# Optimization experiments

Hardware: AMD Instinct MI355X
Metric: run time of the kernel (lower is better)

The kernel has to match this reference:

```python
import jax, jax.numpy as jnp
import numpy as np

N = 50000
D = 256
E = 800000


def setup_inputs() -> dict:
    key = jax.random.key(0)
    ks = jax.random.split(key, 8)
    x = jax.random.normal(ks[0], (N, D), dtype=jnp.float32)
    edge_index = jax.random.randint(ks[1], (2, E), 0, N, dtype=jnp.int64)
    s = 1.0 / np.sqrt(D)
    # SAGEConv layer 0 params: lin_l (neighbors, with bias), lin_r (root, no bias)
    Wl0 = jax.random.uniform(ks[2], (D, D), jnp.float32, -s, s)
    bl0 = jnp.zeros((D,), jnp.float32)
    Wr0 = jax.random.uniform(ks[3], (D, D), jnp.float32, -s, s)
    # SAGEConv layer 1 params
    Wl1 = jax.random.uniform(ks[4], (D, D), jnp.float32, -s, s)
    bl1 = jnp.zeros((D,), jnp.float32)
    Wr1 = jax.random.uniform(ks[5], (D, D), jnp.float32, -s, s)
    return {"x": x, "edge_index": edge_index, "Wl0": Wl0, "bl0": bl0, "Wr0": Wr0,
            "Wl1": Wl1, "bl1": bl1, "Wr1": Wr1}


def _sage_conv(x, edge_index, Wl, bl, Wr):
    # PyG SAGEConv, aggr='mean': out = lin_l(mean_{j in N(i)} x_j) + lin_r(x_i)
    src, dst = edge_index[0], edge_index[1]
    msg = x[src]                                            # [E, D] gather
    agg = jax.ops.segment_sum(msg, dst, num_segments=x.shape[0])
    cnt = jax.ops.segment_sum(jnp.ones((edge_index.shape[1],), x.dtype), dst,
                              num_segments=x.shape[0])
    mean = agg / jnp.maximum(cnt, 1.0)[:, None]             # zero-degree -> 0
    return mean @ Wl + bl + x @ Wr


def reference(x, edge_index, Wl0, bl0, Wr0, Wl1, bl1, Wr1):
    negative_slope = 0.5
    target = x  # full-graph path: target nodes = all nodes
    h = x
    # dropout p=0.0 -> identity
    h = _sage_conv(h, edge_index, Wl0, bl0, Wr0)
    h = jnp.where(h >= 0, h, negative_slope * h)
    h = _sage_conv(h, edge_index, Wl1, bl1, Wr1)
    h = jnp.where(h >= 0, h, negative_slope * h)
    return (h, target)
```

## Files before the change

kernel.cpp:

```cpp
#include <hip/hip_runtime.h>
#include <hip/hip_fp8.h>


typedef __attribute__((ext_vector_type(8))) short bf16x8;
typedef __attribute__((ext_vector_type(4))) float f32x4;

__device__ __forceinline__ float bf2f(unsigned short b) {
    union { unsigned u; float f; } x; x.u = ((unsigned)b) << 16; return x.f;
}
__device__ __forceinline__ short f2bf(float f) {
    union { float f; unsigned u; } x; x.f = f;
    unsigned r = x.u + 0x7fffu + ((x.u >> 16) & 1u);
    return (short)(r >> 16);
}
__device__ __forceinline__ unsigned char f2fp8(float f) {
    __hip_fp8_e4m3 q(f);
    return (unsigned char)q.__x;
}
__device__ __forceinline__ float fp82f(unsigned char b) {
    __hip_fp8_e4m3 q; q.__x = (__hip_fp8_storage_t)b;
    return (float)q;
}

#define BINA_CHUNK 8192


__global__ __launch_bounds__(512) void bkhist_prep_kernel(
    const int* __restrict__ ei, int* __restrict__ hist, int E, int NBK, int NCH,
    const float* __restrict__ x, short* __restrict__ xb,
    unsigned char* __restrict__ xq, float* __restrict__ xcopy,
    const float* __restrict__ Wl0, const float* __restrict__ Wr0,
    const float* __restrict__ Wl1, const float* __restrict__ Wr1,
    short* __restrict__ B1T, short* __restrict__ B2T, int total8) {
    if ((int)blockIdx.x < NCH) {
        __shared__ int h[512];
        int c = blockIdx.x;
        int base_e = c * BINA_CHUNK;
        int nloc = E - base_e;
        if (nloc > BINA_CHUNK) nloc = BINA_CHUNK;
        for (int b = threadIdx.x; b < 512; b += 512) h[b] = 0;
        __syncthreads();
        for (int t = threadIdx.x; t < nloc; t += 512)
            atomicAdd(&h[ei[E + base_e + t] >> 7], 1);
        __syncthreads();
        if ((int)threadIdx.x < NBK) hist[c * 512 + threadIdx.x] = h[threadIdx.x];
    } else {
        int gid = ((int)blockIdx.x - NCH) * 512 + threadIdx.x;
        if (gid < total8) {
            const float* p = x + (size_t)gid * 8;
            float4 v0 = *reinterpret_cast<const float4*>(p);
            float4 v1 = *reinterpret_cast<const float4*>(p + 4);
            bf16x8 t;
            t[0] = f2bf(v0.x); t[1] = f2bf(v0.y); t[2] = f2bf(v0.z); t[3] = f2bf(v0.w);
            t[4] = f2bf(v1.x); t[5] = f2bf(v1.y); t[6] = f2bf(v1.z); t[7] = f2bf(v1.w);
            *reinterpret_cast<bf16x8*>(xb + (size_t)gid * 8) = t;
            uchar4 q0, q1;
            q0.x = f2fp8(v0.x); q0.y = f2fp8(v0.y); q0.z = f2fp8(v0.z); q0.w = f2fp8(v0.w);
            q1.x = f2fp8(v1.x); q1.y = f2fp8(v1.y); q1.z = f2fp8(v1.z); q1.w = f2fp8(v1.w);
            *reinterpret_cast<uchar4*>(xq + (size_t)gid * 8) = q0;
            *reinterpret_cast<uchar4*>(xq + (size_t)gid * 8 + 4) = q1;
            *reinterpret_cast<float4*>(xcopy + (size_t)gid * 8) = v0;
            *reinterpret_cast<float4*>(xcopy + (size_t)gid * 8 + 4) = v1;
        } else {
            int idx = gid - total8;
            if (idx < 262144) {
                int sel = idx >> 17;
                int j = idx & 131071;
                int n = j >> 9;
                int k = j & 511;
                const float* Wl = sel ? Wl1 : Wl0;
                const float* Wr = sel ? Wr1 : Wr0;
                float v = (k < 256) ? Wl[k * 256 + n] : Wr[(k - 256) * 256 + n];
                (sel ? B2T : B1T)[j] = f2bf(v);
            }
        }
    }
}

__global__ __launch_bounds__(512) void bkscan_kernel(
    int* __restrict__ hist, int* __restrict__ bkoff, int* __restrict__ offs,
    int NBK, int NCH, int N, int E) {
    __shared__ int sm[512];
    int b = threadIdx.x;
    int run = 0;
    if (b < NBK) {
        for (int c = 0; c < NCH; ++c) {
            int h = hist[c * 512 + b];
            hist[c * 512 + b] = run;
            run += h;
        }
    }
    sm[b] = run;
    __syncthreads();
    for (int off = 1; off < 512; off <<= 1) {
        int t = (b >= off) ? sm[b - off] : 0;
        __syncthreads();
        sm[b] += t;
        __syncthreads();
    }
    int excl = sm[b] - run;
    if (b < NBK) {
        bkoff[b] = excl;
        for (int c = 0; c < NCH; ++c) hist[c * 512 + b] += excl;
    }
    if (b == 0) {
        bkoff[NBK] = E;
        offs[N] = E;
    }
}


__global__ __launch_bounds__(512) void binA_kernel(
    const int* __restrict__ ei, const int* __restrict__ hist,
    long long* __restrict__ pairs, int E, int NBK) {
    __shared__ int pos[512];
    int c = blockIdx.x;
    if ((int)threadIdx.x < NBK) pos[threadIdx.x] = hist[c * 512 + threadIdx.x];
    __syncthreads();
    int base_e = c * BINA_CHUNK;
    int nloc = E - base_e;
    if (nloc > BINA_CHUNK) nloc = BINA_CHUNK;
    for (int t = threadIdx.x; t < nloc; t += 512) {
        int dst = ei[E + base_e + t];
        int src = ei[base_e + t];
        int p = atomicAdd(&pos[dst >> 7], 1);
        pairs[p] = ((long long)dst << 32) | (unsigned)src;
    }
}


__global__ __launch_bounds__(256) void binB_kernel(
    const long long* __restrict__ pairs, const int* __restrict__ bkoff,
    int* __restrict__ offs, float* __restrict__ invdeg,
    int* __restrict__ csr, int NBK, int N) {
    __shared__ int cnt[128];
    __shared__ int cur[128];
    int b = blockIdx.x;
    int t = threadIdx.x;
    if (t < 128) cnt[t] = 0;
    __syncthreads();
    int beg = bkoff[b];
    int end = bkoff[b + 1];
    for (int i = beg + t; i < end; i += 256)
        atomicAdd(&cnt[((int)(pairs[i] >> 32)) & 127], 1);
    __syncthreads();
    if (t < 64) {
        int c0 = cnt[2 * t], c1 = cnt[2 * t + 1];
        int s = c0 + c1;
        int incl = s;
        #pragma unroll
        for (int d = 1; d < 64; d <<= 1) {
            int x = __shfl_up(incl, d, 64);
            if (t >= d) incl += x;
        }
        int excl = incl - s;
        cur[2 * t] = beg + excl;
        cur[2 * t + 1] = beg + excl + c0;
    }
    __syncthreads();
    if (t < 128) {
        int node = (b << 7) + t;
        if (node < N) {
            offs[node] = cur[t];
            invdeg[node] = 1.0f / (float)(cnt[t] > 0 ? cnt[t] : 1);
        }
    }
    __syncthreads();
    for (int i = beg + t; i < end; i += 256) {
        long long p = pairs[i];
        int pos = atomicAdd(&cur[((int)(p >> 32)) & 127], 1);
        csr[pos] = (int)(p & 0xffffffffLL);
    }
}

__global__ __launch_bounds__(256) void agg_kernel(
    const unsigned char* __restrict__ feat,
    const int* __restrict__ offs, const int* __restrict__ csr,
    const float* __restrict__ invdeg,
    short* __restrict__ outp, int N) {
    int wave = threadIdx.x >> 6;
    int lane = threadIdx.x & 63;
    int node = blockIdx.x * 4 + wave;
    if (node >= N) return;
    int beg = offs[node];
    int end = offs[node + 1];
    int c = lane * 4;

    float a[4][4];
    #pragma unroll
    for (int u = 0; u < 4; ++u)
        #pragma unroll
        for (int k = 0; k < 4; ++k) a[u][k] = 0.f;

    int deg = end - beg;
    int n8 = deg & ~7;
    for (int t = 0; t < n8; t += 8) {
        int s0 = csr[beg + t];     int s1 = csr[beg + t + 1];
        int s2 = csr[beg + t + 2]; int s3 = csr[beg + t + 3];
        int s4 = csr[beg + t + 4]; int s5 = csr[beg + t + 5];
        int s6 = csr[beg + t + 6]; int s7 = csr[beg + t + 7];
        unsigned u0 = *reinterpret_cast<const unsigned*>(feat + (size_t)s0 * 256 + c);
        unsigned u1 = *reinterpret_cast<const unsigned*>(feat + (size_t)s1 * 256 + c);
        unsigned u2 = *reinterpret_cast<const unsigned*>(feat + (size_t)s2 * 256 + c);
        unsigned u3 = *reinterpret_cast<const unsigned*>(feat + (size_t)s3 * 256 + c);
        unsigned u4 = *reinterpret_cast<const unsigned*>(feat + (size_t)s4 * 256 + c);
        unsigned u5 = *reinterpret_cast<const unsigned*>(feat + (size_t)s5 * 256 + c);
        unsigned u6 = *reinterpret_cast<const unsigned*>(feat + (size_t)s6 * 256 + c);
        unsigned u7 = *reinterpret_cast<const unsigned*>(feat + (size_t)s7 * 256 + c);
        #pragma unroll
        for (int k = 0; k < 4; ++k) a[0][k] += fp82f((u0 >> (8 * k)) & 0xff);
        #pragma unroll
        for (int k = 0; k < 4; ++k) a[1][k] += fp82f((u1 >> (8 * k)) & 0xff);
        #pragma unroll
        for (int k = 0; k < 4; ++k) a[2][k] += fp82f((u2 >> (8 * k)) & 0xff);
        #pragma unroll
        for (int k = 0; k < 4; ++k) a[3][k] += fp82f((u3 >> (8 * k)) & 0xff);
        #pragma unroll
        for (int k = 0; k < 4; ++k) a[0][k] += fp82f((u4 >> (8 * k)) & 0xff);
        #pragma unroll
        for (int k = 0; k < 4; ++k) a[1][k] += fp82f((u5 >> (8 * k)) & 0xff);
        #pragma unroll
        for (int k = 0; k < 4; ++k) a[2][k] += fp82f((u6 >> (8 * k)) & 0xff);
        #pragma unroll
        for (int k = 0; k < 4; ++k) a[3][k] += fp82f((u7 >> (8 * k)) & 0xff);
    }
    for (int e = beg + n8; e < end; ++e) {
        int s = csr[e];
        unsigned u = *reinterpret_cast<const unsigned*>(feat + (size_t)s * 256 + c);
        #pragma unroll
        for (int k = 0; k < 4; ++k) a[0][k] += fp82f((u >> (8 * k)) & 0xff);
    }
    float inv = invdeg[node];
    short4 o;
    o.x = f2bf((a[0][0] + a[1][0] + a[2][0] + a[3][0]) * inv);
    o.y = f2bf((a[0][1] + a[1][1] + a[2][1] + a[3][1]) * inv);
    o.z = f2bf((a[0][2] + a[1][2] + a[2][2] + a[3][2]) * inv);
    o.w = f2bf((a[0][3] + a[1][3] + a[2][3] + a[3][3]) * inv);
    *reinterpret_cast<short4*>(&outp[(size_t)node * 256 + c]) = o;
}

template <int OUT_MODE>
__global__ __launch_bounds__(1024, 4) void gemm_kernel(
    const short* __restrict__ AL, const short* __restrict__ AR,
    const short* __restrict__ BT, const float* __restrict__ bias,
    void* __restrict__ Cout, unsigned char* __restrict__ Cq,
    int M, int ntiles) {
    __shared__ short ldsA[2][32 * 512];
    int wave = threadIdx.x >> 6;
    int lane = threadIdx.x & 63;
    int l16 = lane & 15;
    int lhi = lane >> 4;
    int c0 = wave * 16;

    bf16x8 breg[16];
    #pragma unroll
    for (int kk = 0; kk < 16; ++kk)
        breg[kk] = *reinterpret_cast<const bf16x8*>(
            &BT[(size_t)(c0 + l16) * 512 + kk * 32 + lhi * 8]);
    float bc = bias[c0 + l16];

    auto STAGE = [&](int tt, int buf) {
        #pragma unroll
        for (int i = 0; i < 2; ++i) {
            int r = i * 16 + wave;
            int grow = tt * 32 + r;
            if (grow >= M) grow = M - 1;
            int csw = (lane * 8) ^ ((r & 15) << 3);
            const short* src = (csw < 256)
                ? AL + (size_t)grow * 256 + csw
                : AR + (size_t)grow * 256 + (csw - 256);
            __builtin_amdgcn_global_load_lds(
                (const __attribute__((address_space(1))) unsigned int*)src,
                (__attribute__((address_space(3))) unsigned int*)
                    &ldsA[buf][r * 512],
                16, 0, 0);
        }
    };

    int t = blockIdx.x;
    int stride = gridDim.x;
    if (t >= ntiles) return;
    STAGE(t, 0);
    int buf = 0;
    int it = 0;
    for (; t < ntiles; t += stride, ++it) {
        int tn = t + stride;
        bool havenext = (tn < ntiles);
        if (havenext) STAGE(tn, buf ^ 1);

        if (it == 0) {
            if (havenext) asm volatile("s_waitcnt vmcnt(2)" ::: "memory");
            else          asm volatile("s_waitcnt vmcnt(0)" ::: "memory");
        } else if (havenext) {
            if constexpr (OUT_MODE == 0)
                asm volatile("s_waitcnt vmcnt(18)" ::: "memory");
            else
                asm volatile("s_waitcnt vmcnt(10)" ::: "memory");
        } else {
            if constexpr (OUT_MODE == 0)
                asm volatile("s_waitcnt vmcnt(16)" ::: "memory");
            else
                asm volatile("s_waitcnt vmcnt(8)" ::: "memory");
        }
        __builtin_amdgcn_s_barrier();
        __builtin_amdgcn_sched_barrier(0);

        int row0 = t * 32;
        f32x4 acc[2];
        acc[0] = (f32x4){0.f, 0.f, 0.f, 0.f};
        acc[1] = (f32x4){0.f, 0.f, 0.f, 0.f};

        const short* lb = &ldsA[buf][0];
        #pragma unroll
        for (int kk = 0; kk < 16; ++kk) {
            bf16x8 a0, a1;
            {
                int r = l16;
                int ks = (kk * 32 + lhi * 8) ^ ((r & 15) << 3);
                a0 = *reinterpret_cast<const bf16x8*>(&lb[r * 512 + ks]);
            }
            {
                int r = 16 + l16;
                int ks = (kk * 32 + lhi * 8) ^ ((r & 15) << 3);
                a1 = *reinterpret_cast<const bf16x8*>(&lb[r * 512 + ks]);
            }
            acc[0] = __builtin_amdgcn_mfma_f32_16x16x32_bf16(
                a0, breg[kk], acc[0], 0, 0, 0);
            acc[1] = __builtin_amdgcn_mfma_f32_16x16x32_bf16(
                a1, breg[kk], acc[1], 0, 0, 0);
        }

        #pragma unroll
        for (int mt = 0; mt < 2; ++mt) {
            #pragma unroll
            for (int r = 0; r < 4; ++r) {
                int grow = row0 + mt * 16 + lhi * 4 + r;
                if (grow >= M) grow = M - 1;
                int gcol = c0 + l16;
                float v = acc[mt][r] + bc;
                v = (v >= 0.f) ? v : 0.5f * v;
                if (OUT_MODE == 0) {
                    ((short*)Cout)[(size_t)grow * 256 + gcol] = f2bf(v);
                    Cq[(size_t)grow * 256 + gcol] = f2fp8(v);
                } else {
                    ((float*)Cout)[(size_t)grow * 256 + gcol] = v;
                }
            }
        }
        __builtin_amdgcn_s_barrier();
        buf ^= 1;
    }
}


extern "C" void kernel_launch(void* const* d_in, const int* in_sizes, int n_in,
                              void* d_out, int out_size, void* d_ws, size_t ws_size,
                              hipStream_t stream) {
    const float* x   = (const float*)d_in[0];
    const int*   ei  = (const int*)d_in[1];
    const float* Wl0 = (const float*)d_in[2];
    const float* bl0 = (const float*)d_in[3];
    const float* Wr0 = (const float*)d_in[4];
    const float* Wl1 = (const float*)d_in[5];
    const float* bl1 = (const float*)d_in[6];
    const float* Wr1 = (const float*)d_in[7];

    const int N = in_sizes[0] / 256;
    const int E = in_sizes[1] / 2;
    const int NBK = (N + 127) / 128;
    const int NCH = (E + BINA_CHUNK - 1) / BINA_CHUNK;

    char* ws = (char*)d_ws;
    size_t o = 0;
    auto alloc = [&](size_t bytes) {
        size_t p = o;
        o = (o + bytes + 255) & ~(size_t)255;
        return p;
    };
    int*   offs   = (int*)  (ws + alloc((size_t)(N + 1) * 4));
    float* invdeg = (float*)(ws + alloc((size_t)N * 4));
    int*   hist   = (int*)  (ws + alloc((size_t)NCH * 512 * 4));
    int*   bkoff  = (int*)  (ws + alloc(((size_t)NBK + 1) * 4));
    long long* pairs = (long long*)(ws + alloc((size_t)E * 8));
    int*   csr    = (int*)  (ws + alloc((size_t)E * 4));
    short* xb     = (short*)(ws + alloc((size_t)N * 256 * 2));
    short* meanb  = (short*)(ws + alloc((size_t)N * 256 * 2));
    short* h0     = (short*)(ws + alloc((size_t)N * 256 * 2));
    unsigned char* xq  = (unsigned char*)(ws + alloc((size_t)N * 256));
    unsigned char* h0q = (unsigned char*)(ws + alloc((size_t)N * 256));
    short* B1T    = (short*)(ws + alloc(262144));
    short* B2T    = (short*)(ws + alloc(262144));

    int total8 = N * 32;
    int prep_blocks = (total8 + 262144 + 511) / 512;
    bkhist_prep_kernel<<<NCH + prep_blocks, 512, 0, stream>>>(
        ei, hist, E, NBK, NCH,
        x, xb, xq, (float*)d_out + (size_t)N * 256,
        Wl0, Wr0, Wl1, Wr1, B1T, B2T, total8);
    bkscan_kernel<<<1, 512, 0, stream>>>(hist, bkoff, offs, NBK, NCH, N, E);
    binA_kernel<<<NCH, 512, 0, stream>>>(ei, hist, pairs, E, NBK);
    binB_kernel<<<NBK, 256, 0, stream>>>(pairs, bkoff, offs, invdeg, csr, NBK, N);

    int ab = (N + 3) / 4;
    int ntiles = (N + 31) / 32;
    int gblocks = 512;
    agg_kernel<<<ab, 256, 0, stream>>>(xq, offs, csr, invdeg, meanb, N);
    gemm_kernel<0><<<gblocks, 1024, 0, stream>>>(
        meanb, xb, B1T, bl0, h0, h0q, N, ntiles);
    agg_kernel<<<ab, 256, 0, stream>>>(h0q, offs, csr, invdeg, meanb, N);
    gemm_kernel<1><<<gblocks, 1024, 0, stream>>>(
        meanb, h0, B2T, bl1, d_out, nullptr, N, ntiles);
}
```

Before: 252.2 us.

## Parallelize bucket histogram scan with transposed layout and wave-level scans

Replaces the single-block serial scan over chunks, where each thread looped over NCH entries with strided global reads, with a two-stage scan. The histogram is now stored transposed (bucket-major), one wavefront scans each bucket's chunk counts with shuffles, and a small block scans the bucket totals. binA adds the bucket offset when it loads its positions. This removes a serial latency-bound step at the cost of one extra kernel launch, and the chunk count is capped at 128 by growing the chunk size.

```diff
diff --git a/kernel.cpp b/kernel.cpp
--- a/kernel.cpp
+++ b/kernel.cpp
@@ -22,11 +22,10 @@
     return (float)q;
 }
 
-#define BINA_CHUNK 8192
-
 
 __global__ __launch_bounds__(512) void bkhist_prep_kernel(
-    const int* __restrict__ ei, int* __restrict__ hist, int E, int NBK, int NCH,
+    const int* __restrict__ ei, int* __restrict__ histT,
+    int E, int NBK, int NCH, int CH,
     const float* __restrict__ x, short* __restrict__ xb,
     unsigned char* __restrict__ xq, float* __restrict__ xcopy,
     const float* __restrict__ Wl0, const float* __restrict__ Wr0,
@@ -35,15 +34,15 @@
     if ((int)blockIdx.x < NCH) {
         __shared__ int h[512];
         int c = blockIdx.x;
-        int base_e = c * BINA_CHUNK;
+        int base_e = c * CH;
         int nloc = E - base_e;
-        if (nloc > BINA_CHUNK) nloc = BINA_CHUNK;
-        for (int b = threadIdx.x; b < 512; b += 512) h[b] = 0;
+        if (nloc > CH) nloc = CH;
+        h[threadIdx.x] = 0;
         __syncthreads();
         for (int t = threadIdx.x; t < nloc; t += 512)
             atomicAdd(&h[ei[E + base_e + t] >> 7], 1);
         __syncthreads();
-        if ((int)threadIdx.x < NBK) hist[c * 512 + threadIdx.x] = h[threadIdx.x];
+        if ((int)threadIdx.x < NBK) histT[threadIdx.x * 128 + c] = h[threadIdx.x];
     } else {
         int gid = ((int)blockIdx.x - NCH) * 512 + threadIdx.x;
         if (gid < total8) {
@@ -77,49 +76,66 @@
     }
 }
 
-__global__ __launch_bounds__(512) void bkscan_kernel(
-    int* __restrict__ hist, int* __restrict__ bkoff, int* __restrict__ offs,
-    int NBK, int NCH, int N, int E) {
+__global__ __launch_bounds__(256) void scanA_kernel(
+    int* __restrict__ histT, int* __restrict__ bktot, int NBK, int NCH) {
+    int waveid = blockIdx.x * 4 + (threadIdx.x >> 6);
+    int lane = threadIdx.x & 63;
+    if (waveid >= NBK) return;
+    int b = waveid;
+    int v0 = (lane < NCH) ? histT[b * 128 + lane] : 0;
+    int v1 = (64 + lane < NCH) ? histT[b * 128 + 64 + lane] : 0;
+    int s0 = v0;
+    #pragma unroll
+    for (int d = 1; d < 64; d <<= 1) {
+        int t = __shfl_up(s0, d, 64);
+        if (lane >= d) s0 += t;
+    }
+    int t0 = __shfl(s0, 63, 64);
+    int s1 = v1;
+    #pragma unroll
+    for (int d = 1; d < 64; d <<= 1) {
+        int t = __shfl_up(s1, d, 64);
+        if (lane >= d) s1 += t;
+    }
+    s1 += t0;
+    if (lane < NCH) histT[b * 128 + lane] = s0 - v0;
+    if (64 + lane < NCH) histT[b * 128 + 64 + lane] = s1 - v1;
+    if (lane == 63) bktot[b] = __shfl(s1, 63, 64);
+}
+
+__global__ __launch_bounds__(512) void scanB_kernel(
+    const int* __restrict__ bktot, int* __restrict__ bkoff,
+    int* __restrict__ offs, int NBK, int N, int E) {
     __shared__ int sm[512];
-    int b = threadIdx.x;
-    int run = 0;
-    if (b < NBK) {
-        for (int c = 0; c < NCH; ++c) {
-            int h = hist[c * 512 + b];
-            hist[c * 512 + b] = run;
-            run += h;
-        }
-    }
-    sm[b] = run;
+    int tid = threadIdx.x;
+    int v = (tid < NBK) ? bktot[tid] : 0;
+    sm[tid] = v;
     __syncthreads();
     for (int off = 1; off < 512; off <<= 1) {
-        int t = (b >= off) ? sm[b - off] : 0;
+        int t = (tid >= off) ? sm[tid - off] : 0;
         __syncthreads();
-        sm[b] += t;
+        sm[tid] += t;
         __syncthreads();
     }
-    int excl = sm[b] - run;
-    if (b < NBK) {
-        bkoff[b] = excl;
-        for (int c = 0; c < NCH; ++c) hist[c * 512 + b] += excl;
-    }
-    if (b == 0) {
+    if (tid < NBK) bkoff[tid] = sm[tid] - v;
+    if (tid == 0) {
         bkoff[NBK] = E;
         offs[N] = E;
     }
 }
 
-
 __global__ __launch_bounds__(512) void binA_kernel(
-    const int* __restrict__ ei, const int* __restrict__ hist,
-    long long* __restrict__ pairs, int E, int NBK) {
+    const int* __restrict__ ei, const int* __restrict__ histT,
+    const int* __restrict__ bkoff, long long* __restrict__ pairs,
+    int E, int NBK, int CH) {
     __shared__ int pos[512];
     int c = blockIdx.x;
-    if ((int)threadIdx.x < NBK) pos[threadIdx.x] = hist[c * 512 + threadIdx.x];
-    __syncthreads();
-    int base_e = c * BINA_CHUNK;
+    if ((int)threadIdx.x < NBK)
+        pos[threadIdx.x] = histT[threadIdx.x * 128 + c] + bkoff[threadIdx.x];
+    __syncthreads();
+    int base_e = c * CH;
     int nloc = E - base_e;
-    if (nloc > BINA_CHUNK) nloc = BINA_CHUNK;
+    if (nloc > CH) nloc = CH;
     for (int t = threadIdx.x; t < nloc; t += 512) {
         int dst = ei[E + base_e + t];
         int src = ei[base_e + t];
@@ -127,7 +143,6 @@
         pairs[p] = ((long long)dst << 32) | (unsigned)src;
     }
 }
-
 
 __global__ __launch_bounds__(256) void binB_kernel(
     const long long* __restrict__ pairs, const int* __restrict__ bkoff,
@@ -368,7 +383,9 @@
     const int N = in_sizes[0] / 256;
     const int E = in_sizes[1] / 2;
     const int NBK = (N + 127) / 128;
-    const int NCH = (E + BINA_CHUNK - 1) / BINA_CHUNK;
+    int CH = 8192;
+    while ((E + CH - 1) / CH > 128) CH <<= 1;
+    const int NCH = (E + CH - 1) / CH;
 
     char* ws = (char*)d_ws;
     size_t o = 0;
@@ -379,7 +396,8 @@
     };
     int*   offs   = (int*)  (ws + alloc((size_t)(N + 1) * 4));
     float* invdeg = (float*)(ws + alloc((size_t)N * 4));
-    int*   hist   = (int*)  (ws + alloc((size_t)NCH * 512 * 4));
+    int*   histT  = (int*)  (ws + alloc((size_t)512 * 128 * 4));
+    int*   bktot  = (int*)  (ws + alloc(512 * 4));
     int*   bkoff  = (int*)  (ws + alloc(((size_t)NBK + 1) * 4));
     long long* pairs = (long long*)(ws + alloc((size_t)E * 8));
     int*   csr    = (int*)  (ws + alloc((size_t)E * 4));
@@ -394,11 +412,12 @@
     int total8 = N * 32;
     int prep_blocks = (total8 + 262144 + 511) / 512;
     bkhist_prep_kernel<<<NCH + prep_blocks, 512, 0, stream>>>(
-        ei, hist, E, NBK, NCH,
+        ei, histT, E, NBK, NCH, CH,
         x, xb, xq, (float*)d_out + (size_t)N * 256,
         Wl0, Wr0, Wl1, Wr1, B1T, B2T, total8);
-    bkscan_kernel<<<1, 512, 0, stream>>>(hist, bkoff, offs, NBK, NCH, N, E);
-    binA_kernel<<<NCH, 512, 0, stream>>>(ei, hist, pairs, E, NBK);
+    scanA_kernel<<<(NBK + 3) / 4, 256, 0, stream>>>(histT, bktot, NBK, NCH);
+    scanB_kernel<<<1, 512, 0, stream>>>(bktot, bkoff, offs, NBK, N, E);
+    binA_kernel<<<NCH, 512, 0, stream>>>(ei, histT, bkoff, pairs, E, NBK, CH);
     binB_kernel<<<NBK, 256, 0, stream>>>(pairs, bkoff, offs, invdeg, csr, NBK, N);
 
     int ab = (N + 3) / 4;
```

Result: faster. 219.4 us (-13.0%).
